# Kernel tuning notes

Hardware: AMD Instinct MI355X
Metric: run time of the kernel (lower is better)

The kernel has to match this reference:

```python
import jax, jax.numpy as jnp
import numpy as np
import math

B, S, D, H, F = 2, 2048, 1024, 16, 4096
DK = D // H
NEG_INF = -1000000000.0
EPS = 1e-5


def _layernorm(x, gamma, beta):
    # Faithful to source: torch.std default is unbiased (ddof=1), eps added to std
    mn = jnp.mean(x, axis=-1, keepdims=True)
    sd = jnp.std(x, axis=-1, keepdims=True, ddof=1)
    return (x - mn) / (sd + EPS) * gamma + beta


def _mha(xq, xkv, wq, bq, wk, bk, wv, bv, wo, bo, causal):
    b, sq, d = xq.shape
    sk = xkv.shape[1]
    q = (xq @ wq + bq).reshape(b, sq, H, DK).transpose(0, 2, 1, 3)   # [B,H,Sq,DK]
    k = (xkv @ wk + bk).reshape(b, sk, H, DK).transpose(0, 2, 1, 3)
    v = (xkv @ wv + bv).reshape(b, sk, H, DK).transpose(0, 2, 1, 3)
    scores = jnp.einsum('bhqd,bhkd->bhqk', q, k) / math.sqrt(DK)
    if causal:
        mask = jnp.triu(jnp.ones((sq, sk), dtype=scores.dtype), 1) * NEG_INF
        scores = scores + mask
    w = jax.nn.softmax(scores, axis=-1)
    att = jnp.einsum('bhqk,bhkd->bhqd', w, v).transpose(0, 2, 1, 3).reshape(b, sq, d)
    return att @ wo + bo


def setup_inputs() -> dict:
    key = jax.random.key(0)
    ks = jax.random.split(key, 32)
    it = iter(range(32))

    def lin(din, dout):
        kw = ks[next(it)]
        w = jax.random.normal(kw, (din, dout), jnp.float32) / math.sqrt(din)
        b = jnp.zeros((dout,), jnp.float32)
        return w, b

    X = jax.random.normal(ks[next(it)], (B, S, D), jnp.float32)
    y = jax.random.normal(ks[next(it)], (B, S, D), jnp.float32)
    wq1, bq1 = lin(D, D); wk1, bk1 = lin(D, D); wv1, bv1 = lin(D, D); wo1, bo1 = lin(D, D)
    wq2, bq2 = lin(D, D); wk2, bk2 = lin(D, D); wv2, bv2 = lin(D, D); wo2, bo2 = lin(D, D)
    wf1, bf1 = lin(D, F); wf2, bf2 = lin(F, D)
    g1 = jnp.ones((D,), jnp.float32); be1 = jnp.zeros((D,), jnp.float32)
    g2 = jnp.ones((D,), jnp.float32); be2 = jnp.zeros((D,), jnp.float32)
    g3 = jnp.ones((D,), jnp.float32); be3 = jnp.zeros((D,), jnp.float32)
    return dict(X=X, y=y,
                wq1=wq1, bq1=bq1, wk1=wk1, bk1=bk1, wv1=wv1, bv1=bv1, wo1=wo1, bo1=bo1,
                wq2=wq2, bq2=bq2, wk2=wk2, bk2=bk2, wv2=wv2, bv2=bv2, wo2=wo2, bo2=bo2,
                wf1=wf1, bf1=bf1, wf2=wf2, bf2=bf2,
                g1=g1, be1=be1, g2=g2, be2=be2, g3=g3, be3=be3)


def reference(X, y,
              wq1, bq1, wk1, bk1, wv1, bv1, wo1, bo1,
              wq2, bq2, wk2, bk2, wv2, bv2, wo2, bo2,
              wf1, bf1, wf2, bf2,
              g1, be1, g2, be2, g3, be3):
    # masked self-attention on decoder stream y (dropout = identity at inference)
    res = y
    out = _mha(y, y, wq1, bq1, wk1, bk1, wv1, bv1, wo1, bo1, causal=True)
    out = _layernorm(out + res, g1, be1)
    # cross-attention: queries from decoder, keys/values from encoder X
    res = out
    out = _mha(out, X, wq2, bq2, wk2, bk2, wv2, bv2, wo2, bo2, causal=False)
    out = _layernorm(out + res, g2, be2)
    # feed-forward (ReLU per intended semantics of the source)
    res = out
    out = jax.nn.relu(out @ wf1 + bf1) @ wf2 + bf2
    out = _layernorm(out + res, g3, be3)
    return out
```

## Files before the change

### kernel.cpp

```cpp
#include <hip/hip_runtime.h>

#define DEV __device__ __forceinline__

typedef __attribute__((ext_vector_type(8))) short short8;
typedef __attribute__((ext_vector_type(4))) short s16x4;
typedef __attribute__((ext_vector_type(4))) float f32x4;
typedef __attribute__((ext_vector_type(4))) unsigned u32x4;

DEV unsigned short f2b(float f){
  unsigned r;
  asm("v_cvt_pk_bf16_f32 %0, %1, %1" : "=v"(r) : "v"(f));
  return (unsigned short)r;
}
DEV unsigned cvt_pk2(float lo, float hi){
  unsigned r;
  asm("v_cvt_pk_bf16_f32 %0, %1, %2" : "=v"(r) : "v"(lo), "v"(hi));
  return r;
}
DEV float b2f(unsigned short u){ unsigned v = ((unsigned)u)<<16; float f; __builtin_memcpy(&f,&v,4); return f; }

DEV void gload_lds16(const void* g, void* l){
  __builtin_amdgcn_global_load_lds((const __attribute__((address_space(1))) void*)g,
                                   (__attribute__((address_space(3))) void*)l, 16, 0, 0);
}

#define SCL 0.18033688011112042f

__global__ __launch_bounds__(256) void cvt_f32_bf16(
    const float* __restrict__ in, unsigned short* __restrict__ out, int n)
{
  int i = (blockIdx.x*256 + threadIdx.x)*4;
  if (i >= n) return;
  float4 v = *(const float4*)(in + i);
  uint2 o;
  o.x = cvt_pk2(v.x, v.y);
  o.y = cvt_pk2(v.z, v.w);
  *(uint2*)(out + i) = o;
}

__global__ __launch_bounds__(256) void transpose_cvt(
    const float* __restrict__ W, unsigned short* __restrict__ Wt, int K, int N)
{
  __shared__ float tile[32][33];
  int n0 = blockIdx.x*32, k0 = blockIdx.y*32;
  int tx = threadIdx.x & 31, ty = threadIdx.x >> 5;
  #pragma unroll
  for (int j=0;j<32;j+=8)
    tile[ty+j][tx] = W[(size_t)(k0+ty+j)*N + n0+tx];
  __syncthreads();
  #pragma unroll
  for (int j=0;j<32;j+=8)
    Wt[(size_t)(n0+ty+j)*K + k0+tx] = f2b(tile[tx][ty+j]);
}

template<int EPI>
__global__ __launch_bounds__(256) void gemm_bt(
    const unsigned short* __restrict__ A,
    const unsigned short* __restrict__ Bt,
    const float* __restrict__ bias,
    unsigned short* __restrict__ C,
    int M, int N, int Kc, int LDA, int LDB)
{
  __shared__ alignas(16) unsigned short Asm_[128*32];
  __shared__ alignas(16) unsigned short Bsm_[128*32];
  const int tid = threadIdx.x;
  const int wave = tid>>6, lane = tid&63;
  const int r0 = lane&15, kq = (lane>>4)*8, cq = lane>>4;
  const int m0 = blockIdx.y*128, n0 = blockIdx.x*128;
  const int wr = wave>>1, wc = wave&1;
  const int koff = blockIdx.z * Kc;
  const bool addb = (blockIdx.z == 0);
  C += (size_t)blockIdx.z * M * N;

  f32x4 zero4 = {0.f,0.f,0.f,0.f};
  f32x4 acc[4][4];
  #pragma unroll
  for (int m=0;m<4;m++)
    #pragma unroll
    for (int n=0;n<4;n++) acc[m][n]=zero4;

  const int nk = Kc>>5;
  for (int kt=0; kt<nk; kt++){
    #pragma unroll
    for (int i=0;i<2;i++){
      int idx = i*256 + tid;
      int row = idx>>2, kc = (idx&3)<<3;
      gload_lds16(A  + (size_t)(m0+row)*LDA + koff + (kt<<5) + kc,
                  Asm_ + (size_t)(i*256 + wave*64)*8);
      gload_lds16(Bt + (size_t)(n0+row)*LDB + koff + (kt<<5) + kc,
                  Bsm_ + (size_t)(i*256 + wave*64)*8);
    }
    __syncthreads();
    short8 a[4], b[4];
    #pragma unroll
    for (int m=0;m<4;m++) a[m] = *(const short8*)&Asm_[(wr*64 + m*16 + r0)*32 + kq];
    #pragma unroll
    for (int n=0;n<4;n++) b[n] = *(const short8*)&Bsm_[(wc*64 + n*16 + r0)*32 + kq];
    #pragma unroll
    for (int m=0;m<4;m++)
      #pragma unroll
      for (int n=0;n<4;n++)
        acc[m][n] = __builtin_amdgcn_mfma_f32_16x16x32_bf16(a[m], b[n], acc[m][n], 0,0,0);
    __syncthreads();
  }

  #pragma unroll
  for (int n=0;n<4;n++){
    int col = n0 + wc*64 + n*16 + r0;
    float bs = addb ? bias[col] : 0.f;
    #pragma unroll
    for (int m=0;m<4;m++){
      int rowb = m0 + wr*64 + m*16 + cq*4;
      #pragma unroll
      for (int reg=0;reg<4;reg++){
        float v = acc[m][n][reg] + bs;
        if (EPI==1) v = fmaxf(v, 0.f);
        C[(size_t)(rowb+reg)*N + col] = f2b(v);
      }
    }
  }
}

struct QKVArgs { const float* bias[3]; unsigned short* out[3]; };
template<int NW>
__global__ __launch_bounds__(256) void gemm_qkv(
    const unsigned short* __restrict__ A,
    const unsigned short* __restrict__ Bt,
    QKVArgs args, int M, int K)
{
  __shared__ alignas(16) unsigned short Asm_[128*32];
  __shared__ alignas(16) unsigned short Bsm_[128*32];
  const int tid = threadIdx.x;
  const int wave = tid>>6, lane = tid&63;
  const int r0 = lane&15, kq = (lane>>4)*8, cq = lane>>4;
  const int m0 = blockIdx.y*128, n0 = blockIdx.x*128;
  const int wr = wave>>1, wc = wave&1;

  f32x4 zero4 = {0.f,0.f,0.f,0.f};
  f32x4 acc[4][4];
  #pragma unroll
  for (int m=0;m<4;m++)
    #pragma unroll
    for (int n=0;n<4;n++) acc[m][n]=zero4;

  const int nk = K>>5;
  for (int kt=0; kt<nk; kt++){
    #pragma unroll
    for (int i=0;i<2;i++){
      int idx = i*256 + tid;
      int row = idx>>2, kc = (idx&3)<<3;
      gload_lds16(A  + (size_t)(m0+row)*K + (kt<<5) + kc,
                  Asm_ + (size_t)(i*256 + wave*64)*8);
      gload_lds16(Bt + (size_t)(n0+row)*K + (kt<<5) + kc,
                  Bsm_ + (size_t)(i*256 + wave*64)*8);
    }
    __syncthreads();
    short8 a[4], b[4];
    #pragma unroll
    for (int m=0;m<4;m++) a[m] = *(const short8*)&Asm_[(wr*64 + m*16 + r0)*32 + kq];
    #pragma unroll
    for (int n=0;n<4;n++) b[n] = *(const short8*)&Bsm_[(wc*64 + n*16 + r0)*32 + kq];
    #pragma unroll
    for (int m=0;m<4;m++)
      #pragma unroll
      for (int n=0;n<4;n++)
        acc[m][n] = __builtin_amdgcn_mfma_f32_16x16x32_bf16(a[m], b[n], acc[m][n], 0,0,0);
    __syncthreads();
  }

  const int which = n0>>10;
  const int n0l = n0 & 1023;
  unsigned short* __restrict__ Cout = args.out[which];
  const float* __restrict__ bp = args.bias[which];
  const bool isV = (which == NW-1);
  const float scl = (NW==3 && which==0) ? SCL : 1.f;

  #pragma unroll
  for (int n=0;n<4;n++){
    int col = n0l + wc*64 + n*16 + r0;
    float bs = bp[col];
    int h_ = col>>6, dk = col&63;
    #pragma unroll
    for (int m=0;m<4;m++){
      int rowb = m0 + wr*64 + m*16 + cq*4;
      #pragma unroll
      for (int reg=0;reg<4;reg++){
        float v = (acc[m][n][reg] + bs) * scl;
        int row = rowb + reg;
        int b_ = row>>11, s_ = row&2047;
        if (isV)
          Cout[(((size_t)(b_*16+h_))*64 + dk)*2048 + s_] = f2b(v);
        else
          Cout[(((size_t)(b_*16+h_))*2048 + s_)*64 + dk] = f2b(v);
      }
    }
  }
}

__global__ __launch_bounds__(256) void gemm64q(
    const unsigned short* __restrict__ A,
    const unsigned short* __restrict__ Bt,
    const float* __restrict__ bias,
    unsigned short* __restrict__ C,
    int M, int N, int K)
{
  __shared__ alignas(16) unsigned short Asm_[64*32];
  __shared__ alignas(16) unsigned short Bsm_[128*32];
  const int tid = threadIdx.x;
  const int wave = tid>>6, lane = tid&63;
  const int r0 = lane&15, kq = (lane>>4)*8, cq = lane>>4;
  const int m0 = blockIdx.y*64, n0 = blockIdx.x*128;
  const int wr = wave>>1, wc = wave&1;

  f32x4 zero4 = {0.f,0.f,0.f,0.f};
  f32x4 acc[2][4];
  #pragma unroll
  for (int m=0;m<2;m++)
    #pragma unroll
    for (int n=0;n<4;n++) acc[m][n]=zero4;

  const int nk = K>>5;
  for (int kt=0; kt<nk; kt++){
    {
      int row = tid>>2, kc = (tid&3)<<3;
      gload_lds16(A  + (size_t)(m0+row)*K + (kt<<5) + kc, Asm_ + (size_t)(wave*64)*8);
      gload_lds16(Bt + (size_t)(n0+row)*K + (kt<<5) + kc, Bsm_ + (size_t)(wave*64)*8);
      int idx1 = 256 + tid;
      int row1 = idx1>>2, kc1 = (idx1&3)<<3;
      gload_lds16(Bt + (size_t)(n0+row1)*K + (kt<<5) + kc1, Bsm_ + (size_t)(256 + wave*64)*8);
    }
    __syncthreads();
    short8 a[2], b[4];
    #pragma unroll
    for (int m=0;m<2;m++) a[m] = *(const short8*)&Asm_[(wr*32 + m*16 + r0)*32 + kq];
    #pragma unroll
    for (int n=0;n<4;n++) b[n] = *(const short8*)&Bsm_[(wc*64 + n*16 + r0)*32 + kq];
    #pragma unroll
    for (int m=0;m<2;m++)
      #pragma unroll
      for (int n=0;n<4;n++)
        acc[m][n] = __builtin_amdgcn_mfma_f32_16x16x32_bf16(a[m], b[n], acc[m][n], 0,0,0);
    __syncthreads();
  }

  #pragma unroll
  for (int n=0;n<4;n++){
    int col = n0 + wc*64 + n*16 + r0;
    float bs = bias[col];
    int h_ = col>>6, dk = col&63;
    #pragma unroll
    for (int m=0;m<2;m++){
      int rowb = m0 + wr*32 + m*16 + cq*4;
      #pragma unroll
      for (int reg=0;reg<4;reg++){
        float v = (acc[m][n][reg] + bs) * SCL;
        int row = rowb + reg;
        int b_ = row>>11, s_ = row&2047;
        C[(((size_t)(b_*16+h_))*2048 + s_)*64 + dk] = f2b(v);
      }
    }
  }
}

template<int MODE>
__global__ __launch_bounds__(256, 4) void attn_kernel(
    const unsigned short* __restrict__ Q,
    const unsigned short* __restrict__ K,
    const unsigned short* __restrict__ Vt,
    unsigned short* __restrict__ O,
    float* __restrict__ po, float* __restrict__ ml)
{
  __shared__ alignas(16) unsigned short Ksm[2][64*64];
  __shared__ alignas(16) unsigned short Vsm[2][64*64];
  const int S = 2048, DK = 64;
  const int h = blockIdx.y, b = blockIdx.z;
  const int tid = threadIdx.x, wave = tid>>6, lane = tid&63;
  const int r0 = lane&15, kq = (lane>>4)*8, cq = lane>>4;

  int qb, t0, t1, chunk = 0;
  bool partial = false;
  if (MODE==1){
    int bx = blockIdx.x;
    if (bx < 32){ qb = bx; t0 = 0; t1 = (qb<15?qb:15); chunk = 0; partial = (qb>=16); }
    else        { qb = bx-16; t0 = 16; t1 = qb; chunk = 1; partial = true; }
  } else { qb = blockIdx.x; t0 = 0; t1 = S/64 - 1; }

  const unsigned short* qh = Q  + ((size_t)(b*16+h))*S*DK;
  const unsigned short* kh = K  + ((size_t)(b*16+h))*S*DK;
  const unsigned short* vh = Vt + ((size_t)(b*16+h))*DK*S;

  const int idx0 = tid, idx1 = 256 + tid;
  const int rr0 = idx0>>3, cc0 = (idx0&7)<<3;
  const int rr1 = idx1>>3, cc1 = (idx1&7)<<3;
  const int sw0 = (idx0*8) ^ ((rr0&7)<<3);
  const int sw1 = (idx1*8) ^ ((rr1&7)<<3);
  const int swr = (r0&7)<<3;

  short8 qa[2];
  {
    int qrow = qb*64 + wave*16 + r0;
    qa[0] = *(const short8*)&qh[(size_t)qrow*DK + kq];
    qa[1] = *(const short8*)&qh[(size_t)qrow*DK + 32 + kq];
  }

  f32x4 zero4 = {0.f,0.f,0.f,0.f};
  f32x4 o[4];
  float mr = -INFINITY, lr = 0.f;
  #pragma unroll
  for (int n=0;n<4;n++) o[n]=zero4;

  short8 kr0, kr1, vr0, vr1;
  kr0 = *(const short8*)&kh[(size_t)(t0*64+rr0)*DK + cc0];
  kr1 = *(const short8*)&kh[(size_t)(t0*64+rr1)*DK + cc1];
  vr0 = *(const short8*)&vh[(size_t)rr0*S + t0*64 + cc0];
  vr1 = *(const short8*)&vh[(size_t)rr1*S + t0*64 + cc1];
  *(short8*)&Ksm[0][sw0] = kr0;
  *(short8*)&Ksm[0][sw1] = kr1;
  *(short8*)&Vsm[0][sw0] = vr0;
  *(short8*)&Vsm[0][sw1] = vr1;
  __syncthreads();

  int cur = 0;
  for (int t=t0; t<=t1; t++){
    const bool pf = (t < t1);
    if (pf){
      kr0 = *(const short8*)&kh[(size_t)((t+1)*64+rr0)*DK + cc0];
      kr1 = *(const short8*)&kh[(size_t)((t+1)*64+rr1)*DK + cc1];
      vr0 = *(const short8*)&vh[(size_t)rr0*S + (t+1)*64 + cc0];
      vr1 = *(const short8*)&vh[(size_t)rr1*S + (t+1)*64 + cc1];
    }

    f32x4 sv[4];
    #pragma unroll
    for (int n=0;n<4;n++) sv[n]=zero4;
    #pragma unroll
    for (int n=0;n<4;n++)
      #pragma unroll
      for (int kk=0;kk<2;kk++){
        short8 kb = *(const short8*)&Ksm[cur][(((n*16 + r0)*64) + kk*32 + kq) ^ swr];
        sv[n] = __builtin_amdgcn_mfma_f32_16x16x32_bf16(kb, qa[kk], sv[n], 0,0,0);
      }
    if (MODE==1 && t==qb){
      const int qg = wave*16 + r0;
      #pragma unroll
      for (int n=0;n<4;n++)
        #pragma unroll
        for (int reg=0;reg<4;reg++){
          if (n*16 + cq*4 + reg > qg) sv[n][reg] += -1000000000.0f;
        }
    }

    float m2 = fmaxf(fmaxf(fmaxf(sv[0][0],sv[0][1]),fmaxf(sv[0][2],sv[0][3])),
               fmaxf(fmaxf(fmaxf(sv[1][0],sv[1][1]),fmaxf(sv[1][2],sv[1][3])),
               fmaxf(fmaxf(fmaxf(sv[2][0],sv[2][1]),fmaxf(sv[2][2],sv[2][3])),
                     fmaxf(fmaxf(sv[3][0],sv[3][1]),fmaxf(sv[3][2],sv[3][3])))));
    m2 = fmaxf(m2, __shfl_xor(m2, 16, 64));
    m2 = fmaxf(m2, __shfl_xor(m2, 32, 64));
    bool need = (m2 > mr + 8.f);
    if (__ballot(need)){
      float nm = fmaxf(mr, m2);
      float fac = exp2f(mr - nm);
      mr = nm; lr *= fac;
      #pragma unroll
      for (int n=0;n<4;n++) o[n] *= fac;
    }
    float ps = 0.f;
    #pragma unroll
    for (int n=0;n<4;n++)
      #pragma unroll
      for (int reg=0;reg<4;reg++){
        float p = exp2f(sv[n][reg] - mr);
        sv[n][reg] = p; ps += p;
      }
    ps += __shfl_xor(ps, 16, 64);
    ps += __shfl_xor(ps, 32, 64);
    lr += ps;

    short8 pa[2];
    #pragma unroll
    for (int kk=0;kk<2;kk++){
      u32x4 w;
      w[0] = cvt_pk2(sv[2*kk][0],   sv[2*kk][1]);
      w[1] = cvt_pk2(sv[2*kk][2],   sv[2*kk][3]);
      w[2] = cvt_pk2(sv[2*kk+1][0], sv[2*kk+1][1]);
      w[3] = cvt_pk2(sv[2*kk+1][2], sv[2*kk+1][3]);
      pa[kk] = __builtin_bit_cast(short8, w);
    }

    #pragma unroll
    for (int n=0;n<4;n++)
      #pragma unroll
      for (int kk=0;kk<2;kk++){
        int base = (n*16 + r0)*64 + kk*32 + cq*4;
        s16x4 lo = *(const s16x4*)&Vsm[cur][base ^ swr];
        s16x4 hi = *(const s16x4*)&Vsm[cur][(base + 16) ^ swr];
        short8 vb = __builtin_shufflevector(lo, hi, 0,1,2,3,4,5,6,7);
        o[n] = __builtin_amdgcn_mfma_f32_16x16x32_bf16(vb, pa[kk], o[n], 0,0,0);
      }

    if (pf){
      *(short8*)&Ksm[cur^1][sw0] = kr0;
      *(short8*)&Ksm[cur^1][sw1] = kr1;
      *(short8*)&Vsm[cur^1][sw0] = vr0;
      *(short8*)&Vsm[cur^1][sw1] = vr1;
    }
    __syncthreads();
    cur ^= 1;
  }

  if (MODE==1 && partial){
    float* pop = po + (size_t)chunk*2097152;
    float* mlp = ml + (size_t)chunk*65536;
    const int bh = b*16 + h, qb16 = qb - 16;
    const int rowIdx = (bh*16 + qb16)*64 + wave*16 + r0;
    if (cq == 0){ mlp[rowIdx*2] = mr; mlp[rowIdx*2+1] = lr; }
    #pragma unroll
    for (int n=0;n<4;n++){
      float4 v; v.x=o[n][0]; v.y=o[n][1]; v.z=o[n][2]; v.w=o[n][3];
      *(float4*)&pop[(size_t)rowIdx*64 + n*16 + cq*4] = v;
    }
  } else {
    const int sg = qb*64 + wave*16 + r0;
    const float inv = 1.f / lr;
    unsigned short* op = O + ((size_t)b*S + sg)*1024 + h*64;
    #pragma unroll
    for (int n=0;n<4;n++){
      uint2 w;
      w.x = cvt_pk2(o[n][0]*inv, o[n][1]*inv);
      w.y = cvt_pk2(o[n][2]*inv, o[n][3]*inv);
      *(uint2*)(op + n*16 + cq*4) = w;
    }
  }
}

__global__ __launch_bounds__(256) void attn_merge(
    const float* __restrict__ po, const float* __restrict__ ml,
    unsigned short* __restrict__ O)
{
  int gid = blockIdx.x*256 + threadIdx.x;
  int row = gid>>4, dq = (gid&15)*4;
  float m0 = ml[row*2],          l0 = ml[row*2+1];
  float m1 = ml[65536 + row*2],  l1 = ml[65536 + row*2+1];
  float m = fmaxf(m0, m1);
  float a0 = exp2f(m0 - m), a1 = exp2f(m1 - m);
  float inv = 1.f / (l0*a0 + l1*a1);
  float4 v0 = *(const float4*)(po + (size_t)row*64 + dq);
  float4 v1 = *(const float4*)(po + 2097152 + (size_t)row*64 + dq);
  float r0 = (v0.x*a0 + v1.x*a1)*inv;
  float r1 = (v0.y*a0 + v1.y*a1)*inv;
  float r2 = (v0.z*a0 + v1.z*a1)*inv;
  float r3 = (v0.w*a0 + v1.w*a1)*inv;
  int bh = row>>10, qb16 = (row>>6)&15, qr = row&63;
  int b = bh>>4, h = bh&15;
  int s = (16+qb16)*64 + qr;
  unsigned short* op = O + ((size_t)b*2048 + s)*1024 + h*64 + dq;
  uint2 out; out.x = cvt_pk2(r0, r1); out.y = cvt_pk2(r2, r3);
  *(uint2*)op = out;
}

template<int OUT_F32>
__global__ __launch_bounds__(256) void add_ln3(
    const unsigned short* __restrict__ a0, const unsigned short* __restrict__ a1,
    const unsigned short* __restrict__ r,
    const float* __restrict__ g, const float* __restrict__ be, void* outp)
{
  const int row = blockIdx.x, tid = threadIdx.x;
  const size_t base = (size_t)row*1024 + tid*4;
  ushort4 va = *(const ushort4*)(a0 + base);
  ushort4 vb_ = *(const ushort4*)(a1 + base);
  ushort4 vr = *(const ushort4*)(r + base);
  float x[4];
  x[0] = b2f(va.x)+b2f(vb_.x)+b2f(vr.x);
  x[1] = b2f(va.y)+b2f(vb_.y)+b2f(vr.y);
  x[2] = b2f(va.z)+b2f(vb_.z)+b2f(vr.z);
  x[3] = b2f(va.w)+b2f(vb_.w)+b2f(vr.w);
  float s = x[0]+x[1]+x[2]+x[3];
  float ss = x[0]*x[0]+x[1]*x[1]+x[2]*x[2]+x[3]*x[3];
  #pragma unroll
  for (int d=1;d<64;d<<=1){ s += __shfl_xor(s,d,64); ss += __shfl_xor(ss,d,64); }
  __shared__ float rs[4], rss[4];
  int wave = tid>>6, lane = tid&63;
  if (lane==0){ rs[wave]=s; rss[wave]=ss; }
  __syncthreads();
  s = rs[0]+rs[1]+rs[2]+rs[3];
  ss = rss[0]+rss[1]+rss[2]+rss[3];
  float mean = s*(1.f/1024.f);
  float var = (ss - 1024.f*mean*mean)*(1.f/1023.f);
  float sd = sqrtf(fmaxf(var,0.f));
  float inv = 1.f/(sd + 1e-5f);
  float4 vg = *(const float4*)(g + tid*4);
  float4 vbe = *(const float4*)(be + tid*4);
  float o0 = (x[0]-mean)*inv*vg.x+vbe.x;
  float o1 = (x[1]-mean)*inv*vg.y+vbe.y;
  float o2 = (x[2]-mean)*inv*vg.z+vbe.z;
  float o3 = (x[3]-mean)*inv*vg.w+vbe.w;
  if (OUT_F32){
    float4 vo; vo.x=o0; vo.y=o1; vo.z=o2; vo.w=o3;
    *(float4*)((float*)outp + base) = vo;
  } else {
    uint2 vo; vo.x = cvt_pk2(o0,o1); vo.y = cvt_pk2(o2,o3);
    *(uint2*)((unsigned short*)outp + base) = vo;
  }
}

extern "C" void kernel_launch(void* const* d_in, const int* in_sizes, int n_in,
                              void* d_out, int out_size, void* d_ws, size_t ws_size,
                              hipStream_t stream)
{
  typedef const float* cf;
  cf X   = (cf)d_in[0],  y   = (cf)d_in[1];
  cf wq1 = (cf)d_in[2],  bq1 = (cf)d_in[3],  wk1 = (cf)d_in[4],  bk1 = (cf)d_in[5];
  cf wv1 = (cf)d_in[6],  bv1 = (cf)d_in[7],  wo1 = (cf)d_in[8],  bo1 = (cf)d_in[9];
  cf wq2 = (cf)d_in[10], bq2 = (cf)d_in[11], wk2 = (cf)d_in[12], bk2 = (cf)d_in[13];
  cf wv2 = (cf)d_in[14], bv2 = (cf)d_in[15], wo2 = (cf)d_in[16], bo2 = (cf)d_in[17];
  cf wf1 = (cf)d_in[18], bf1 = (cf)d_in[19], wf2 = (cf)d_in[20], bf2 = (cf)d_in[21];
  cf g1  = (cf)d_in[22], be1 = (cf)d_in[23], g2  = (cf)d_in[24], be2 = (cf)d_in[25];
  cf g3  = (cf)d_in[26], be3 = (cf)d_in[27];

  char* ws = (char*)d_ws;
  const size_t MB = 1u<<20;
  unsigned short* wq1t = (unsigned short*)(ws + 0*MB);
  unsigned short* wk1t = (unsigned short*)(ws + 2*MB);
  unsigned short* wv1t = (unsigned short*)(ws + 4*MB);
  unsigned short* wo1t = (unsigned short*)(ws + 6*MB);
  unsigned short* wq2t = (unsigned short*)(ws + 8*MB);
  unsigned short* wk2t = (unsigned short*)(ws + 10*MB);
  unsigned short* wv2t = (unsigned short*)(ws + 12*MB);
  unsigned short* wo2t = (unsigned short*)(ws + 14*MB);
  unsigned short* wf1t = (unsigned short*)(ws + 16*MB);
  unsigned short* wf2t = (unsigned short*)(ws + 24*MB);
  unsigned short* Qb   = (unsigned short*)(ws + 32*MB);
  unsigned short* Kb   = (unsigned short*)(ws + 40*MB);
  unsigned short* Vtb  = (unsigned short*)(ws + 48*MB);
  unsigned short* attno= (unsigned short*)(ws + 56*MB);
  unsigned short* hbuf = (unsigned short*)(ws + 32*MB);
  unsigned short* part = (unsigned short*)(ws + 64*MB);
  float*          poF  = (float*)(ws + 64*MB);
  float*          mlF  = (float*)(ws + 80*MB);
  unsigned short* x1b  = (unsigned short*)(ws + 80*MB);
  unsigned short* slot = (unsigned short*)(ws + 88*MB);
  unsigned short* yb = slot, *Xb = slot, *x2b = slot;

  dim3 blk(256);
  const int NTOK = 2*2048*1024;
  cvt_f32_bf16<<<NTOK/1024, blk, 0, stream>>>(y, yb, NTOK);

  dim3 tsq(32,32), tf1(128,32), tf2(32,128);
  transpose_cvt<<<tsq, blk, 0, stream>>>(wq1, wq1t, 1024, 1024);
  transpose_cvt<<<tsq, blk, 0, stream>>>(wk1, wk1t, 1024, 1024);
  transpose_cvt<<<tsq, blk, 0, stream>>>(wv1, wv1t, 1024, 1024);
  transpose_cvt<<<tsq, blk, 0, stream>>>(wo1, wo1t, 1024, 1024);
  transpose_cvt<<<tsq, blk, 0, stream>>>(wq2, wq2t, 1024, 1024);
  transpose_cvt<<<tsq, blk, 0, stream>>>(wk2, wk2t, 1024, 1024);
  transpose_cvt<<<tsq, blk, 0, stream>>>(wv2, wv2t, 1024, 1024);
  transpose_cvt<<<tsq, blk, 0, stream>>>(wo2, wo2t, 1024, 1024);
  transpose_cvt<<<tf1, blk, 0, stream>>>(wf1, wf1t, 1024, 4096);
  transpose_cvt<<<tf2, blk, 0, stream>>>(wf2, wf2t, 4096, 1024);

  dim3 gqkv(24,32);
  dim3 gkv(16,32);
  dim3 gq2(8,64);
  dim3 gs(8,32,2);
  dim3 gff1(32,32,1);
  dim3 gac(48,16,2);
  dim3 gax(32,16,2);

  {
    QKVArgs a1; a1.bias[0]=bq1; a1.bias[1]=bk1; a1.bias[2]=bv1;
    a1.out[0]=Qb; a1.out[1]=Kb; a1.out[2]=Vtb;
    gemm_qkv<3><<<gqkv, blk, 0, stream>>>(yb, wq1t, a1, 4096, 1024);
  }
  attn_kernel<1><<<gac, blk, 0, stream>>>(Qb, Kb, Vtb, attno, poF, mlF);
  attn_merge<<<2048, blk, 0, stream>>>(poF, mlF, attno);
  gemm_bt<0><<<gs, blk, 0, stream>>>(attno, wo1t, bo1, part, 4096, 1024, 512, 1024, 1024);
  add_ln3<0><<<4096, blk, 0, stream>>>(part, part+4194304, yb, g1, be1, x1b);

  cvt_f32_bf16<<<NTOK/1024, blk, 0, stream>>>(X, Xb, NTOK);
  gemm64q<<<gq2, blk, 0, stream>>>(x1b, wq2t, bq2, Qb, 4096, 1024, 1024);
  {
    QKVArgs a2; a2.bias[0]=bk2; a2.bias[1]=bv2; a2.bias[2]=nullptr;
    a2.out[0]=Kb; a2.out[1]=Vtb; a2.out[2]=nullptr;
    gemm_qkv<2><<<gkv, blk, 0, stream>>>(Xb, wk2t, a2, 4096, 1024);
  }
  attn_kernel<0><<<gax, blk, 0, stream>>>(Qb, Kb, Vtb, attno, nullptr, nullptr);
  gemm_bt<0><<<gs, blk, 0, stream>>>(attno, wo2t, bo2, part, 4096, 1024, 512, 1024, 1024);
  add_ln3<0><<<4096, blk, 0, stream>>>(part, part+4194304, x1b, g2, be2, x2b);

  gemm_bt<1><<<gff1, blk, 0, stream>>>(x2b, wf1t, bf1, hbuf, 4096, 4096, 1024, 1024, 1024);
  gemm_bt<0><<<gs, blk, 0, stream>>>(hbuf, wf2t, bf2, part, 4096, 1024, 2048, 4096, 4096);
  add_ln3<1><<<4096, blk, 0, stream>>>(part, part+4194304, x2b, g3, be3, d_out);
}
```

Measured before the change: 459.0 us.

## Batch weight transposes, fuse cross-attn QKV GEMM, split cross-attn KV range

Replaces the ten separate weight transpose launches with a single batched launch indexed by blockIdx.z. Merges the cross-attention Q projection and K/V projection into one gemm_qkv launch by giving each output third its own A pointer. Splits the cross-attention KV range into two chunks, doubling the grid, writes bf16 partials plus max/sum stats, and adds a merge kernel. It also raises the attention launch-bounds occupancy hint from 4 to 5. The goal is to cut launch overhead and fill the GPU better, at the cost of extra partial-output traffic, a merge pass, and bf16 rounding of partials.

```diff
diff --git a/kernel.cpp b/kernel.cpp
--- a/kernel.cpp
+++ b/kernel.cpp
@@ -38,11 +38,21 @@
   *(uint2*)(out + i) = o;
 }
 
-__global__ __launch_bounds__(256) void transpose_cvt(
-    const float* __restrict__ W, unsigned short* __restrict__ Wt, int K, int N)
-{
+struct TransAll {
+  const float* W[10]; unsigned short* Wt[10];
+  int K[10], N[10], swapxy[10];
+};
+__global__ __launch_bounds__(256) void transpose_cvt_all(TransAll p)
+{
+  const int z = blockIdx.z;
+  const int bx = p.swapxy[z] ? blockIdx.y : blockIdx.x;
+  const int by = p.swapxy[z] ? blockIdx.x : blockIdx.y;
+  const int K = p.K[z], N = p.N[z];
+  const int n0 = bx*32, k0 = by*32;
+  if (n0 >= N || k0 >= K) return;
+  const float* __restrict__ W = p.W[z];
+  unsigned short* __restrict__ Wt = p.Wt[z];
   __shared__ float tile[32][33];
-  int n0 = blockIdx.x*32, k0 = blockIdx.y*32;
   int tx = threadIdx.x & 31, ty = threadIdx.x >> 5;
   #pragma unroll
   for (int j=0;j<32;j+=8)
@@ -121,10 +131,8 @@
   }
 }
 
-struct QKVArgs { const float* bias[3]; unsigned short* out[3]; };
-template<int NW>
+struct QKVArgs { const unsigned short* Aw[3]; const float* bias[3]; unsigned short* out[3]; };
 __global__ __launch_bounds__(256) void gemm_qkv(
-    const unsigned short* __restrict__ A,
     const unsigned short* __restrict__ Bt,
     QKVArgs args, int M, int K)
 {
@@ -135,6 +143,8 @@
   const int r0 = lane&15, kq = (lane>>4)*8, cq = lane>>4;
   const int m0 = blockIdx.y*128, n0 = blockIdx.x*128;
   const int wr = wave>>1, wc = wave&1;
+  const int which = n0>>10;
+  const unsigned short* __restrict__ A = args.Aw[which];
 
   f32x4 zero4 = {0.f,0.f,0.f,0.f};
   f32x4 acc[4][4];
@@ -168,12 +178,11 @@
     __syncthreads();
   }
 
-  const int which = n0>>10;
   const int n0l = n0 & 1023;
   unsigned short* __restrict__ Cout = args.out[which];
   const float* __restrict__ bp = args.bias[which];
-  const bool isV = (which == NW-1);
-  const float scl = (NW==3 && which==0) ? SCL : 1.f;
+  const bool isV = (which == 2);
+  const float scl = (which == 0) ? SCL : 1.f;
 
   #pragma unroll
   for (int n=0;n<4;n++){
@@ -197,78 +206,14 @@
   }
 }
 
-__global__ __launch_bounds__(256) void gemm64q(
-    const unsigned short* __restrict__ A,
-    const unsigned short* __restrict__ Bt,
-    const float* __restrict__ bias,
-    unsigned short* __restrict__ C,
-    int M, int N, int K)
-{
-  __shared__ alignas(16) unsigned short Asm_[64*32];
-  __shared__ alignas(16) unsigned short Bsm_[128*32];
-  const int tid = threadIdx.x;
-  const int wave = tid>>6, lane = tid&63;
-  const int r0 = lane&15, kq = (lane>>4)*8, cq = lane>>4;
-  const int m0 = blockIdx.y*64, n0 = blockIdx.x*128;
-  const int wr = wave>>1, wc = wave&1;
-
-  f32x4 zero4 = {0.f,0.f,0.f,0.f};
-  f32x4 acc[2][4];
-  #pragma unroll
-  for (int m=0;m<2;m++)
-    #pragma unroll
-    for (int n=0;n<4;n++) acc[m][n]=zero4;
-
-  const int nk = K>>5;
-  for (int kt=0; kt<nk; kt++){
-    {
-      int row = tid>>2, kc = (tid&3)<<3;
-      gload_lds16(A  + (size_t)(m0+row)*K + (kt<<5) + kc, Asm_ + (size_t)(wave*64)*8);
-      gload_lds16(Bt + (size_t)(n0+row)*K + (kt<<5) + kc, Bsm_ + (size_t)(wave*64)*8);
-      int idx1 = 256 + tid;
-      int row1 = idx1>>2, kc1 = (idx1&3)<<3;
-      gload_lds16(Bt + (size_t)(n0+row1)*K + (kt<<5) + kc1, Bsm_ + (size_t)(256 + wave*64)*8);
-    }
-    __syncthreads();
-    short8 a[2], b[4];
-    #pragma unroll
-    for (int m=0;m<2;m++) a[m] = *(const short8*)&Asm_[(wr*32 + m*16 + r0)*32 + kq];
-    #pragma unroll
-    for (int n=0;n<4;n++) b[n] = *(const short8*)&Bsm_[(wc*64 + n*16 + r0)*32 + kq];
-    #pragma unroll
-    for (int m=0;m<2;m++)
-      #pragma unroll
-      for (int n=0;n<4;n++)
-        acc[m][n] = __builtin_amdgcn_mfma_f32_16x16x32_bf16(a[m], b[n], acc[m][n], 0,0,0);
-    __syncthreads();
-  }
-
-  #pragma unroll
-  for (int n=0;n<4;n++){
-    int col = n0 + wc*64 + n*16 + r0;
-    float bs = bias[col];
-    int h_ = col>>6, dk = col&63;
-    #pragma unroll
-    for (int m=0;m<2;m++){
-      int rowb = m0 + wr*32 + m*16 + cq*4;
-      #pragma unroll
-      for (int reg=0;reg<4;reg++){
-        float v = (acc[m][n][reg] + bs) * SCL;
-        int row = rowb + reg;
-        int b_ = row>>11, s_ = row&2047;
-        C[(((size_t)(b_*16+h_))*2048 + s_)*64 + dk] = f2b(v);
-      }
-    }
-  }
-}
-
 template<int MODE>
-__global__ __launch_bounds__(256, 4) void attn_kernel(
+__global__ __launch_bounds__(256, 5) void attn_kernel(
     const unsigned short* __restrict__ Q,
     const unsigned short* __restrict__ K,
     const unsigned short* __restrict__ Vt,
     unsigned short* __restrict__ O,
-    float* __restrict__ po, float* __restrict__ ml)
+    float* __restrict__ po, unsigned short* __restrict__ pob,
+    float* __restrict__ ml)
 {
   __shared__ alignas(16) unsigned short Ksm[2][64*64];
   __shared__ alignas(16) unsigned short Vsm[2][64*64];
@@ -283,7 +228,12 @@
     int bx = blockIdx.x;
     if (bx < 32){ qb = bx; t0 = 0; t1 = (qb<15?qb:15); chunk = 0; partial = (qb>=16); }
     else        { qb = bx-16; t0 = 16; t1 = qb; chunk = 1; partial = true; }
-  } else { qb = blockIdx.x; t0 = 0; t1 = S/64 - 1; }
+  } else {
+    int bx = blockIdx.x;
+    if (bx < 32){ qb = bx; t0 = 0; t1 = 15; chunk = 0; }
+    else        { qb = bx-32; t0 = 16; t1 = 31; chunk = 1; }
+    partial = true;
+  }
 
   const unsigned short* qh = Q  + ((size_t)(b*16+h))*S*DK;
   const unsigned short* kh = K  + ((size_t)(b*16+h))*S*DK;
@@ -418,6 +368,19 @@
     for (int n=0;n<4;n++){
       float4 v; v.x=o[n][0]; v.y=o[n][1]; v.z=o[n][2]; v.w=o[n][3];
       *(float4*)&pop[(size_t)rowIdx*64 + n*16 + cq*4] = v;
+    }
+  } else if (MODE==2){
+    unsigned short* pop = pob + (size_t)chunk*4194304;
+    float* mlp = ml + (size_t)chunk*131072;
+    const int bh = b*16 + h;
+    const int rowIdx = (bh*32 + qb)*64 + wave*16 + r0;
+    if (cq == 0){ mlp[rowIdx*2] = mr; mlp[rowIdx*2+1] = lr; }
+    #pragma unroll
+    for (int n=0;n<4;n++){
+      uint2 w;
+      w.x = cvt_pk2(o[n][0], o[n][1]);
+      w.y = cvt_pk2(o[n][2], o[n][3]);
+      *(uint2*)(pop + (size_t)rowIdx*64 + n*16 + cq*4) = w;
     }
   } else {
     const int sg = qb*64 + wave*16 + r0;
@@ -453,6 +416,30 @@
   int bh = row>>10, qb16 = (row>>6)&15, qr = row&63;
   int b = bh>>4, h = bh&15;
   int s = (16+qb16)*64 + qr;
+  unsigned short* op = O + ((size_t)b*2048 + s)*1024 + h*64 + dq;
+  uint2 out; out.x = cvt_pk2(r0, r1); out.y = cvt_pk2(r2, r3);
+  *(uint2*)op = out;
+}
+
+__global__ __launch_bounds__(256) void attn_merge_x(
+    const unsigned short* __restrict__ pob, const float* __restrict__ ml,
+    unsigned short* __restrict__ O)
+{
+  int gid = blockIdx.x*256 + threadIdx.x;
+  int row = gid>>4, dq = (gid&15)*4;
+  float m0 = ml[row*2],           l0 = ml[row*2+1];
+  float m1 = ml[131072 + row*2],  l1 = ml[131072 + row*2+1];
+  float m = fmaxf(m0, m1);
+  float a0 = exp2f(m0 - m), a1 = exp2f(m1 - m);
+  float inv = 1.f / (l0*a0 + l1*a1);
+  ushort4 u0 = *(const ushort4*)(pob + (size_t)row*64 + dq);
+  ushort4 u1 = *(const ushort4*)(pob + 4194304 + (size_t)row*64 + dq);
+  float r0 = (b2f(u0.x)*a0 + b2f(u1.x)*a1)*inv;
+  float r1 = (b2f(u0.y)*a0 + b2f(u1.y)*a1)*inv;
+  float r2 = (b2f(u0.z)*a0 + b2f(u1.z)*a1)*inv;
+  float r3 = (b2f(u0.w)*a0 + b2f(u1.w)*a1)*inv;
+  int bh = row>>11, s = row&2047;
+  int b = bh>>4, h = bh&15;
   unsigned short* op = O + ((size_t)b*2048 + s)*1024 + h*64 + dq;
   uint2 out; out.x = cvt_pk2(r0, r1); out.y = cvt_pk2(r2, r3);
   *(uint2*)op = out;
@@ -536,53 +523,58 @@
   unsigned short* hbuf = (unsigned short*)(ws + 32*MB);
   unsigned short* part = (unsigned short*)(ws + 64*MB);
   float*          poF  = (float*)(ws + 64*MB);
+  unsigned short* pobF = (unsigned short*)(ws + 64*MB);
   float*          mlF  = (float*)(ws + 80*MB);
   unsigned short* x1b  = (unsigned short*)(ws + 80*MB);
   unsigned short* slot = (unsigned short*)(ws + 88*MB);
   unsigned short* yb = slot, *Xb = slot, *x2b = slot;
+  float*          mlX  = (float*)(ws + 88*MB);
 
   dim3 blk(256);
   const int NTOK = 2*2048*1024;
   cvt_f32_bf16<<<NTOK/1024, blk, 0, stream>>>(y, yb, NTOK);
 
-  dim3 tsq(32,32), tf1(128,32), tf2(32,128);
-  transpose_cvt<<<tsq, blk, 0, stream>>>(wq1, wq1t, 1024, 1024);
-  transpose_cvt<<<tsq, blk, 0, stream>>>(wk1, wk1t, 1024, 1024);
-  transpose_cvt<<<tsq, blk, 0, stream>>>(wv1, wv1t, 1024, 1024);
-  transpose_cvt<<<tsq, blk, 0, stream>>>(wo1, wo1t, 1024, 1024);
-  transpose_cvt<<<tsq, blk, 0, stream>>>(wq2, wq2t, 1024, 1024);
-  transpose_cvt<<<tsq, blk, 0, stream>>>(wk2, wk2t, 1024, 1024);
-  transpose_cvt<<<tsq, blk, 0, stream>>>(wv2, wv2t, 1024, 1024);
-  transpose_cvt<<<tsq, blk, 0, stream>>>(wo2, wo2t, 1024, 1024);
-  transpose_cvt<<<tf1, blk, 0, stream>>>(wf1, wf1t, 1024, 4096);
-  transpose_cvt<<<tf2, blk, 0, stream>>>(wf2, wf2t, 4096, 1024);
+  {
+    TransAll tp;
+    const float* Ws[10]   = {wq1,wk1,wv1,wo1,wq2,wk2,wv2,wo2,wf1,wf2};
+    unsigned short* Ts[10]= {wq1t,wk1t,wv1t,wo1t,wq2t,wk2t,wv2t,wo2t,wf1t,wf2t};
+    for (int i=0;i<10;i++){
+      tp.W[i]=Ws[i]; tp.Wt[i]=Ts[i];
+      tp.K[i] = (i==9)?4096:1024;
+      tp.N[i] = (i==8)?4096:1024;
+      tp.swapxy[i] = (i==9)?1:0;
+    }
+    transpose_cvt_all<<<dim3(128,32,10), blk, 0, stream>>>(tp);
+  }
 
   dim3 gqkv(24,32);
-  dim3 gkv(16,32);
-  dim3 gq2(8,64);
   dim3 gs(8,32,2);
   dim3 gff1(32,32,1);
   dim3 gac(48,16,2);
-  dim3 gax(32,16,2);
+  dim3 gax(64,16,2);
 
   {
-    QKVArgs a1; a1.bias[0]=bq1; a1.bias[1]=bk1; a1.bias[2]=bv1;
+    QKVArgs a1;
+    a1.Aw[0]=yb; a1.Aw[1]=yb; a1.Aw[2]=yb;
+    a1.bias[0]=bq1; a1.bias[1]=bk1; a1.bias[2]=bv1;
     a1.out[0]=Qb; a1.out[1]=Kb; a1.out[2]=Vtb;
-    gemm_qkv<3><<<gqkv, blk, 0, stream>>>(yb, wq1t, a1, 4096, 1024);
-  }
-  attn_kernel<1><<<gac, blk, 0, stream>>>(Qb, Kb, Vtb, attno, poF, mlF);
+    gemm_qkv<<<gqkv, blk, 0, stream>>>(wq1t, a1, 4096, 1024);
+  }
+  attn_kernel<1><<<gac, blk, 0, stream>>>(Qb, Kb, Vtb, attno, poF, nullptr, mlF);
   attn_merge<<<2048, blk, 0, stream>>>(poF, mlF, attno);
   gemm_bt<0><<<gs, blk, 0, stream>>>(attno, wo1t, bo1, part, 4096, 1024, 512, 1024, 1024);
   add_ln3<0><<<4096, blk, 0, stream>>>(part, part+4194304, yb, g1, be1, x1b);
 
   cvt_f32_bf16<<<NTOK/1024, blk, 0, stream>>>(X, Xb, NTOK);
-  gemm64q<<<gq2, blk, 0, stream>>>(x1b, wq2t, bq2, Qb, 4096, 1024, 1024);
   {
-    QKVArgs a2; a2.bias[0]=bk2; a2.bias[1]=bv2; a2.bias[2]=nullptr;
-    a2.out[0]=Kb; a2.out[1]=Vtb; a2.out[2]=nullptr;
-    gemm_qkv<2><<<gkv, blk, 0, stream>>>(Xb, wk2t, a2, 4096, 1024);
-  }
-  attn_kernel<0><<<gax, blk, 0, stream>>>(Qb, Kb, Vtb, attno, nullptr, nullptr);
+    QKVArgs a2;
+    a2.Aw[0]=x1b; a2.Aw[1]=Xb; a2.Aw[2]=Xb;
+    a2.bias[0]=bq2; a2.bias[1]=bk2; a2.bias[2]=bv2;
+    a2.out[0]=Qb; a2.out[1]=Kb; a2.out[2]=Vtb;
+    gemm_qkv<<<gqkv, blk, 0, stream>>>(wq2t, a2, 4096, 1024);
+  }
+  attn_kernel<2><<<gax, blk, 0, stream>>>(Qb, Kb, Vtb, attno, nullptr, pobF, mlX);
+  attn_merge_x<<<4096, blk, 0, stream>>>(pobF, mlX, attno);
   gemm_bt<0><<<gs, blk, 0, stream>>>(attno, wo2t, bo2, part, 4096, 1024, 512, 1024, 1024);
   add_ln3<0><<<4096, blk, 0, stream>>>(part, part+4194304, x1b, g2, be2, x2b);
 
```

Measured after the change: 520.9 us. 1.14x slower.
